# Optimization experiments

Measured on AMD Instinct MI355X. Metric: run time of the kernel, lower is better.

Reference implementation:

```python
import jax, jax.numpy as jnp
import numpy as np


def _bitrev_indices(N):
    # bit-reversal permutation, vectorized in numpy (static, N known at trace time)
    bits = int(np.log2(N))
    idx = np.arange(N, dtype=np.int64)
    rev = np.zeros(N, dtype=np.int64)
    for _ in range(bits):
        rev = (rev << 1) | (idx & 1)
        idx >>= 1
    return jnp.asarray(rev)


def setup_inputs() -> dict:
    key = jax.random.key(0)
    k1, k2 = jax.random.split(key)
    B, N = 2048, 4096
    return {
        "x_re": jax.random.normal(k1, (B, N), dtype=jnp.float32),
        "x_im": jax.random.normal(k2, (B, N), dtype=jnp.float32),
    }


def reference(x_re, x_im):
    # Radix-2 decimation-in-time Cooley-Tukey FFT, faithful to PythonFFT.forward
    N = x_re.shape[-1]
    batch = x_re.shape[:-1]
    num_stages = int(np.log2(N))

    # twiddle table W_N^k = exp(-2*pi*i*k/N) (matches compute_twiddle_table)
    k = jnp.arange(N, dtype=jnp.float32)
    angles = (-2.0 * np.pi) * k / N
    W_re_tab = jnp.cos(angles)
    W_im_tab = jnp.sin(angles)

    br = _bitrev_indices(N)
    y_re = x_re[..., br]
    y_im = x_im[..., br]

    # loop over log2(N) stages (small fixed loop); each stage is fully vectorized
    for stage in range(num_stages):
        stride = 1 << stage
        group = stride << 1
        # twiddle index for butterfly position j in a group: j * (N // group) % N
        tw_idx = (jnp.arange(stride) * (N // group)) % N
        w_re = W_re_tab[tw_idx]  # [stride]
        w_im = W_im_tab[tw_idx]  # [stride]

        yr = y_re.reshape(*batch, N // group, 2, stride)
        yi = y_im.reshape(*batch, N // group, 2, stride)
        a_re, b_re = yr[..., 0, :], yr[..., 1, :]
        a_im, b_im = yi[..., 0, :], yi[..., 1, :]

        wb_re = w_re * b_re - w_im * b_im
        wb_im = w_re * b_im + w_im * b_re

        y_re = jnp.stack([a_re + wb_re, a_re - wb_re], axis=-2).reshape(*batch, N)
        y_im = jnp.stack([a_im + wb_im, a_im - wb_im], axis=-2).reshape(*batch, N)

    return (y_re, y_im)
```

## Files before the change

### kernel.cpp

```cpp
#include <hip/hip_runtime.h>
#include <math.h>

#define FFT_N   4096
#define THREADS 256
#define RPB     4
#define RH 0.70710678118654752f
#define C16 0.92387953251128676f
#define S16 0.38268343236508977f
#define NEG2PI_256  (-2.45436926061702597e-2f)
#define NEG2PI_4096 (-1.53398078788564123e-3f)

#define POS(k) ((((k) & 3) << 2) | ((k) >> 2))

__device__ __forceinline__ float2 cmul(float2 a, float2 b) {
    return make_float2(a.x * b.x - a.y * b.y, a.x * b.y + a.y * b.x);
}

__device__ __forceinline__ void bar_lds() {
    asm volatile("s_waitcnt lgkmcnt(0)\n\ts_barrier" ::: "memory");
}

__device__ __forceinline__ void dft4(float2& a, float2& b, float2& c, float2& d) {
    float2 t0 = make_float2(a.x + c.x, a.y + c.y);
    float2 t1 = make_float2(a.x - c.x, a.y - c.y);
    float2 t2 = make_float2(b.x + d.x, b.y + d.y);
    float2 t3 = make_float2(b.y - d.y, d.x - b.x);
    a = make_float2(t0.x + t2.x, t0.y + t2.y);
    b = make_float2(t1.x + t3.x, t1.y + t3.y);
    c = make_float2(t0.x - t2.x, t0.y - t2.y);
    d = make_float2(t1.x - t3.x, t1.y - t3.y);
}

template<int E>
__device__ __forceinline__ float2 mw16(float2 z) {
    if constexpr (E == 0) return z;
    else if constexpr (E == 4) return make_float2(z.y, -z.x);
    else if constexpr (E == 2) return make_float2(RH * (z.x + z.y), RH * (z.y - z.x));
    else if constexpr (E == 6) return make_float2(RH * (z.y - z.x), -RH * (z.x + z.y));
    else if constexpr (E == 1) return cmul(z, make_float2(C16, -S16));
    else if constexpr (E == 3) return cmul(z, make_float2(S16, -C16));
    else           return cmul(z, make_float2(-C16, S16));
}

__device__ __forceinline__ void dft16(float2 (&v)[16]) {
    dft4(v[0], v[4], v[8],  v[12]);
    dft4(v[1], v[5], v[9],  v[13]);
    dft4(v[2], v[6], v[10], v[14]);
    dft4(v[3], v[7], v[11], v[15]);
    v[5]  = mw16<1>(v[5]);   v[9]  = mw16<2>(v[9]);   v[13] = mw16<3>(v[13]);
    v[6]  = mw16<2>(v[6]);   v[10] = mw16<4>(v[10]);  v[14] = mw16<6>(v[14]);
    v[7]  = mw16<3>(v[7]);   v[11] = mw16<6>(v[11]);  v[15] = mw16<9>(v[15]);
    dft4(v[0],  v[1],  v[2],  v[3]);
    dft4(v[4],  v[5],  v[6],  v[7]);
    dft4(v[8],  v[9],  v[10], v[11]);
    dft4(v[12], v[13], v[14], v[15]);
}

template<bool PF>
__device__ __forceinline__ void process_row(
    float2 (&v)[16], float2 (&vn)[16], float2* __restrict__ sd,
    const int t, const int lo, const int hi,
    const float2 (&b)[4], const float2 (&c)[4],
    const float2 (&Pw)[4], const float2 (&zz)[4], const int wb2,
    const float* __restrict__ xr_n, const float* __restrict__ xi_n,
    float* __restrict__ yr, float* __restrict__ yi)
{
    if constexpr (PF) {
        #pragma unroll
        for (int n3 = 0; n3 < 16; ++n3) {
            vn[n3].x = xr_n[t + (n3 << 8)];
            vn[n3].y = xi_n[t + (n3 << 8)];
        }
    }

    dft16(v);

    #pragma unroll
    for (int k3 = 0; k3 < 16; ++k3) {
        float2 z = v[POS(k3)];
        if (k3 & 3)  z = cmul(z, b[k3 & 3]);
        if (k3 >> 2) z = cmul(z, c[k3 >> 2]);
        sd[t + (k3 << 8)] = z;
    }
    bar_lds();

    #pragma unroll
    for (int n2 = 0; n2 < 16; ++n2)
        v[n2] = sd[lo + (n2 << 4) + (hi << 8)];
    bar_lds();

    dft16(v);

    #pragma unroll
    for (int k2 = 0; k2 < 16; ++k2) {
        float2 u = cmul(v[POS(k2)], Pw[k2 & 3]);
        if (k2 >> 2) u = cmul(u, zz[k2 >> 2]);
        sd[wb2 + (k2 << 4)] = u;
    }
    bar_lds();

    #pragma unroll
    for (int m = 0; m < 16; ++m)
        v[m] = sd[(lo ^ m) + (hi << 4) + (m << 8)];

    dft16(v);
    #pragma unroll
    for (int k1 = 0; k1 < 16; ++k1) {
        __builtin_nontemporal_store(v[POS(k1)].x, &yr[t + (k1 << 8)]);
        __builtin_nontemporal_store(v[POS(k1)].y, &yi[t + (k1 << 8)]);
    }
    bar_lds();
}

__global__ __launch_bounds__(THREADS)
void fft4096_pipe(const float* __restrict__ xre, const float* __restrict__ xim,
                  float* __restrict__ yre, float* __restrict__ yim)
{
    __shared__ float2 sd[FFT_N];

    const int t  = threadIdx.x;
    const int lo = t & 15;
    const int hi = t >> 4;

    float2 b[4], c[4], Pw[4], zz[4];
    {
        float sn, cs;
        __sincosf((float)hi * NEG2PI_256, &sn, &cs);
        b[0] = make_float2(1.f, 0.f);
        b[1] = make_float2(cs, sn);
        b[2] = cmul(b[1], b[1]);
        b[3] = cmul(b[2], b[1]);
        c[0] = make_float2(1.f, 0.f);
        c[1] = cmul(b[2], b[2]);
        c[2] = cmul(c[1], c[1]);
        c[3] = cmul(c[2], c[1]);
        __sincosf((float)(lo * hi) * NEG2PI_4096, &sn, &cs);
        const float2 P = make_float2(cs, sn);
        __sincosf((float)lo * NEG2PI_256, &sn, &cs);
        float2 w1 = make_float2(cs, sn);
        float2 w2 = cmul(w1, w1);
        float2 w3 = cmul(w2, w1);
        Pw[0] = P;
        Pw[1] = cmul(P, w1);
        Pw[2] = cmul(P, w2);
        Pw[3] = cmul(P, w3);
        zz[0] = make_float2(1.f, 0.f);
        zz[1] = cmul(w2, w2);
        zz[2] = cmul(zz[1], zz[1]);
        zz[3] = cmul(zz[2], zz[1]);
    }
    const int wb2 = (lo ^ hi) + (lo << 8);

    const size_t r0 = (size_t)blockIdx.x * RPB * FFT_N;
    const float* xr = xre + r0;
    const float* xi = xim + r0;
    float*       yr = yre + r0;
    float*       yi = yim + r0;

    float2 va[16], vb[16];
    #pragma unroll
    for (int n3 = 0; n3 < 16; ++n3) {
        va[n3].x = xr[t + (n3 << 8)];
        va[n3].y = xi[t + (n3 << 8)];
    }

    process_row<true >(va, vb, sd, t, lo, hi, b, c, Pw, zz, wb2,
                       xr + FFT_N,     xi + FFT_N,     yr,             yi);
    process_row<true >(vb, va, sd, t, lo, hi, b, c, Pw, zz, wb2,
                       xr + 2 * FFT_N, xi + 2 * FFT_N, yr + FFT_N,     yi + FFT_N);
    process_row<true >(va, vb, sd, t, lo, hi, b, c, Pw, zz, wb2,
                       xr + 3 * FFT_N, xi + 3 * FFT_N, yr + 2 * FFT_N, yi + 2 * FFT_N);
    process_row<false>(vb, va, sd, t, lo, hi, b, c, Pw, zz, wb2,
                       xr,             xi,             yr + 3 * FFT_N, yi + 3 * FFT_N);
}

extern "C" void kernel_launch(void* const* d_in, const int* in_sizes, int n_in,
                              void* d_out, int out_size, void* d_ws, size_t ws_size,
                              hipStream_t stream) {
    const float* xre = (const float*)d_in[0];
    const float* xim = (const float*)d_in[1];
    const int total = in_sizes[0];
    const int rows  = total / FFT_N;
    float* yre = (float*)d_out;
    float* yim = yre + total;
    fft4096_pipe<<<dim3(rows / RPB), dim3(THREADS), 0, stream>>>(xre, xim, yre, yim);
}
```

Measured before the change: 26.45 us.

## Vectorize global loads/stores to float4 via LDS transposes and deferred stores

Global loads and stores now use float4 accesses instead of scalar strided ones. Data is staged through a padded LDS buffer (bufQ) on input and an XOR-swizzled pass through the existing buffer on output. Output stores for a row are deferred and interleaved into the next row's compute, and the prefetch of the next row is moved later. This adds LDS traffic, extra barriers and a second shared buffer (about 72KB total, with launch bounds requesting 2 blocks per SM), which may reduce occupancy.

```diff
diff --git a/kernel.cpp b/kernel.cpp
--- a/kernel.cpp
+++ b/kernel.cpp
@@ -56,71 +56,115 @@
     dft4(v[12], v[13], v[14], v[15]);
 }
 
-template<bool PF>
+template<bool ST, bool PF>
 __device__ __forceinline__ void process_row(
-    float2 (&v)[16], float2 (&vn)[16], float2* __restrict__ sd,
-    const int t, const int lo, const int hi,
+    float4 (&Lr)[4], float4 (&Li)[4], float2 (&vo)[16],
+    float2* __restrict__ bufQ, float2* __restrict__ buf,
+    const int t, const int lo, const int hi, const int w, const int l,
     const float2 (&b)[4], const float2 (&c)[4],
-    const float2 (&Pw)[4], const float2 (&zz)[4], const int wb2,
-    const float* __restrict__ xr_n, const float* __restrict__ xi_n,
-    float* __restrict__ yr, float* __restrict__ yi)
+    const float2 (&Pw)[4], const float2 (&zz)[4], const int wb2, const int wb3,
+    const float4* __restrict__ xr4_n, const float4* __restrict__ xi4_n,
+    float4* __restrict__ yr4_p, float4* __restrict__ yi4_p)
 {
-    if constexpr (PF) {
-        #pragma unroll
-        for (int n3 = 0; n3 < 16; ++n3) {
-            vn[n3].x = xr_n[t + (n3 << 8)];
-            vn[n3].y = xi_n[t + (n3 << 8)];
-        }
+    #pragma unroll
+    for (int j = 0; j < 4; ++j) {
+        const int base = 320 * (w + 4 * j) + 5 * l;
+        bufQ[base + 0] = make_float2(Lr[j].x, Li[j].x);
+        bufQ[base + 1] = make_float2(Lr[j].y, Li[j].y);
+        bufQ[base + 2] = make_float2(Lr[j].z, Li[j].z);
+        bufQ[base + 3] = make_float2(Lr[j].w, Li[j].w);
+    }
+    if constexpr (ST) {
+        #pragma unroll
+        for (int d = 0; d < 4; ++d)
+            yr4_p[t + (d << 8)] = make_float4(vo[4*d].x, vo[4*d+1].x,
+                                              vo[4*d+2].x, vo[4*d+3].x);
+    }
+    bar_lds();
+
+    float2 v[16];
+    {
+        const int rb = 5 * (t >> 2) + (t & 3);
+        #pragma unroll
+        for (int n3 = 0; n3 < 16; ++n3)
+            v[n3] = bufQ[rb + 320 * n3];
     }
 
     dft16(v);
-
     #pragma unroll
     for (int k3 = 0; k3 < 16; ++k3) {
         float2 z = v[POS(k3)];
         if (k3 & 3)  z = cmul(z, b[k3 & 3]);
         if (k3 >> 2) z = cmul(z, c[k3 >> 2]);
-        sd[t + (k3 << 8)] = z;
+        buf[t + (k3 << 8)] = z;
+    }
+    if constexpr (ST) {
+        #pragma unroll
+        for (int d = 0; d < 4; ++d)
+            yi4_p[t + (d << 8)] = make_float4(vo[4*d].y, vo[4*d+1].y,
+                                              vo[4*d+2].y, vo[4*d+3].y);
     }
     bar_lds();
 
     #pragma unroll
     for (int n2 = 0; n2 < 16; ++n2)
-        v[n2] = sd[lo + (n2 << 4) + (hi << 8)];
-    bar_lds();
+        v[n2] = buf[lo + (n2 << 4) + (hi << 8)];
+    bar_lds();
+
+    if constexpr (PF) {
+        #pragma unroll
+        for (int j = 0; j < 4; ++j) {
+            Lr[j] = xr4_n[t + (j << 8)];
+            Li[j] = xi4_n[t + (j << 8)];
+        }
+    }
 
     dft16(v);
-
     #pragma unroll
     for (int k2 = 0; k2 < 16; ++k2) {
         float2 u = cmul(v[POS(k2)], Pw[k2 & 3]);
         if (k2 >> 2) u = cmul(u, zz[k2 >> 2]);
-        sd[wb2 + (k2 << 4)] = u;
+        buf[wb2 + (k2 << 4)] = u;
     }
     bar_lds();
 
     #pragma unroll
     for (int m = 0; m < 16; ++m)
-        v[m] = sd[(lo ^ m) + (hi << 4) + (m << 8)];
+        v[m] = buf[(lo ^ m) + (hi << 4) + (m << 8)];
 
     dft16(v);
-    #pragma unroll
-    for (int k1 = 0; k1 < 16; ++k1) {
-        __builtin_nontemporal_store(v[POS(k1)].x, &yr[t + (k1 << 8)]);
-        __builtin_nontemporal_store(v[POS(k1)].y, &yi[t + (k1 << 8)]);
-    }
-    bar_lds();
-}
-
-__global__ __launch_bounds__(THREADS)
-void fft4096_pipe(const float* __restrict__ xre, const float* __restrict__ xim,
-                  float* __restrict__ yre, float* __restrict__ yim)
+    bar_lds();
+
+    #pragma unroll
+    for (int k1 = 0; k1 < 16; ++k1)
+        buf[wb3 + (k1 << 8)] = v[POS(k1)];
+    bar_lds();
+
+    {
+        const int x = (t >> 2) & 15;
+        #pragma unroll
+        for (int d = 0; d < 4; ++d) {
+            #pragma unroll
+            for (int m = 0; m < 4; ++m) {
+                const int k = 4 * t + m + (d << 10);
+                vo[4 * d + m] = buf[k ^ x];
+            }
+        }
+    }
+}
+
+__global__ __launch_bounds__(THREADS, 2)
+void fft4096_v4(const float* __restrict__ xre, const float* __restrict__ xim,
+                float* __restrict__ yre, float* __restrict__ yim)
 {
-    __shared__ float2 sd[FFT_N];
+    __shared__ float2 bufQ[5120];
+    __shared__ float2 buf[FFT_N];
 
     const int t  = threadIdx.x;
     const int lo = t & 15;
     const int hi = t >> 4;
+    const int w  = t >> 6;
+    const int l  = t & 63;
 
     float2 b[4], c[4], Pw[4], zz[4];
     {
@@ -150,28 +194,43 @@
         zz[3] = cmul(zz[2], zz[1]);
     }
     const int wb2 = (lo ^ hi) + (lo << 8);
+    const int wb3 = (lo ^ hi) + (hi << 4);
 
     const size_t r0 = (size_t)blockIdx.x * RPB * FFT_N;
-    const float* xr = xre + r0;
-    const float* xi = xim + r0;
-    float*       yr = yre + r0;
-    float*       yi = yim + r0;
-
-    float2 va[16], vb[16];
-    #pragma unroll
-    for (int n3 = 0; n3 < 16; ++n3) {
-        va[n3].x = xr[t + (n3 << 8)];
-        va[n3].y = xi[t + (n3 << 8)];
-    }
-
-    process_row<true >(va, vb, sd, t, lo, hi, b, c, Pw, zz, wb2,
-                       xr + FFT_N,     xi + FFT_N,     yr,             yi);
-    process_row<true >(vb, va, sd, t, lo, hi, b, c, Pw, zz, wb2,
-                       xr + 2 * FFT_N, xi + 2 * FFT_N, yr + FFT_N,     yi + FFT_N);
-    process_row<true >(va, vb, sd, t, lo, hi, b, c, Pw, zz, wb2,
-                       xr + 3 * FFT_N, xi + 3 * FFT_N, yr + 2 * FFT_N, yi + 2 * FFT_N);
-    process_row<false>(vb, va, sd, t, lo, hi, b, c, Pw, zz, wb2,
-                       xr,             xi,             yr + 3 * FFT_N, yi + 3 * FFT_N);
+    const float4* xr4 = (const float4*)(xre + r0);
+    const float4* xi4 = (const float4*)(xim + r0);
+    float4*       yr4 = (float4*)(yre + r0);
+    float4*       yi4 = (float4*)(yim + r0);
+    const int Q = FFT_N / 4;
+
+    float4 Lr[4], Li[4];
+    float2 vo[16];
+    #pragma unroll
+    for (int j = 0; j < 4; ++j) {
+        Lr[j] = xr4[t + (j << 8)];
+        Li[j] = xi4[t + (j << 8)];
+    }
+
+    process_row<false, true >(Lr, Li, vo, bufQ, buf, t, lo, hi, w, l,
+                              b, c, Pw, zz, wb2, wb3,
+                              xr4 + Q,     xi4 + Q,     yr4,         yi4);
+    process_row<true , true >(Lr, Li, vo, bufQ, buf, t, lo, hi, w, l,
+                              b, c, Pw, zz, wb2, wb3,
+                              xr4 + 2 * Q, xi4 + 2 * Q, yr4,         yi4);
+    process_row<true , true >(Lr, Li, vo, bufQ, buf, t, lo, hi, w, l,
+                              b, c, Pw, zz, wb2, wb3,
+                              xr4 + 3 * Q, xi4 + 3 * Q, yr4 + Q,     yi4 + Q);
+    process_row<true , false>(Lr, Li, vo, bufQ, buf, t, lo, hi, w, l,
+                              b, c, Pw, zz, wb2, wb3,
+                              xr4,         xi4,         yr4 + 2 * Q, yi4 + 2 * Q);
+
+    #pragma unroll
+    for (int d = 0; d < 4; ++d) {
+        yr4[3 * Q + t + (d << 8)] = make_float4(vo[4*d].x, vo[4*d+1].x,
+                                                vo[4*d+2].x, vo[4*d+3].x);
+        yi4[3 * Q + t + (d << 8)] = make_float4(vo[4*d].y, vo[4*d+1].y,
+                                                vo[4*d+2].y, vo[4*d+3].y);
+    }
 }
 
 extern "C" void kernel_launch(void* const* d_in, const int* in_sizes, int n_in,
@@ -183,5 +242,5 @@
     const int rows  = total / FFT_N;
     float* yre = (float*)d_out;
     float* yim = yre + total;
-    fft4096_pipe<<<dim3(rows / RPB), dim3(THREADS), 0, stream>>>(xre, xim, yre, yim);
-}
+    fft4096_v4<<<dim3(rows / RPB), dim3(THREADS), 0, stream>>>(xre, xim, yre, yim);
+}
```

New measurement: 28.27 us. 1.07x slower.
